# Kernel optimization log

Measured on AMD Instinct MI355X. Metric: run time of the kernel, lower is better.

## Reference

```python
import jax, jax.numpy as jnp
import numpy as np

SQN = 3      # hardcoded recurrence depth
ATT_H = 256  # hardcoded attention hidden size
STRIDE = 16  # segment length (hardcoded expand(-1,16,-1))


def setup_inputs() -> dict:
    key = jax.random.key(0)
    ks = jax.random.split(key, 12)
    B, Cin, H, V = 64, 512, 512, 512

    def w(k, shape, fan_in):
        return jax.random.normal(k, shape, jnp.float32) / np.sqrt(fan_in).astype(np.float32)

    return {
        "visual_input": jax.random.normal(ks[0], (B, Cin, V), jnp.float32),
        "text_feature": jax.random.normal(ks[1], (B, H), jnp.float32),
        # weights stored [in, out] (transposed vs torch nn.Linear)
        "vis_conv_w": w(ks[2], (Cin, H), Cin),   # 1x1 Conv1d == linear over channels
        "vis_conv_b": jnp.zeros((H,), jnp.float32),
        "glob_w": w(ks[3], (SQN, H, H), H),      # 3 distinct global_emb linears
        "glob_b": jnp.zeros((SQN, H), jnp.float32),
        "guide_w": w(ks[4], (2 * H, H), 2 * H),
        "guide_b": jnp.zeros((H,), jnp.float32),
        "att1_w": w(ks[5], (H, ATT_H), H),
        "att1_b": jnp.zeros((ATT_H,), jnp.float32),
        "att2_w": w(ks[6], (H, ATT_H), H),
        "att2_b": jnp.zeros((ATT_H,), jnp.float32),
        "att3_w": w(ks[7], (ATT_H, 1), ATT_H),
        "att3_b": jnp.zeros((1,), jnp.float32),
        "out_conv_w": w(ks[8], (H, H), H),       # 1x1 Conv1d
        "out_conv_b": jnp.zeros((H,), jnp.float32),
        "text_w": w(ks[9], (H, H), H),
        "text_b": jnp.zeros((H,), jnp.float32),
    }


def reference(visual_input, text_feature, vis_conv_w, vis_conv_b, glob_w, glob_b,
              guide_w, guide_b, att1_w, att1_b, att2_w, att2_b, att3_w, att3_b,
              out_conv_w, out_conv_b, text_w, text_b):
    B, Cin, V = visual_input.shape
    H = vis_conv_w.shape[1]
    S = V // STRIDE  # number of segments

    # vis_conv (1x1) + relu: [B, H, V]
    vis_h = jax.nn.relu(jnp.einsum('bcv,ch->bhv', visual_input, vis_conv_w)
                        + vis_conv_b[None, :, None])
    # split into segments: [B, S, T=16, H]
    vis_seg = vis_h.reshape(B, H, S, STRIDE).transpose(0, 2, 3, 1)
    # AvgPool1d(kernel=stride) == per-segment mean: [B, S, H]
    avg_seg = vis_seg.mean(axis=2)
    # text projection: [B, H]
    text_att = text_feature @ text_w + text_b

    # precompute att_fn2(vis_seg): [B, S, T, ATT_H] (loop-invariant)
    att2_pre = jnp.einsum('bsth,ha->bsta', vis_seg, att2_w) + att2_b

    prev_se = jnp.zeros((B, S, H), vis_seg.dtype)
    se_list, att_list = [], []
    for m in range(SQN):  # fixed 3-step recurrence, distinct weights per step
        v_n = jnp.einsum('bsh,hk->bsk', avg_seg, glob_w[m]) + glob_b[m]
        # guide_emb (Linear+ReLU) followed by an outer relu == single relu
        g_n = jax.nn.relu(jnp.concatenate([v_n, prev_se], axis=-1) @ guide_w + guide_b)
        att = jnp.tanh((g_n @ att1_w + att1_b)[:, :, None, :] + att2_pre)  # [B,S,T,A]
        att = att @ att3_w + att3_b                                        # [B,S,T,1]
        att = jax.nn.softmax(att, axis=2)  # softmax over the 16 frames
        prev_se = jnp.sum(vis_seg * att, axis=2)  # [B, S, H]
        se_list.append(prev_se)
        att_list.append(att)

    vis_for_att = jnp.stack(se_list, axis=2)  # [B, S, 3, H]
    fuse_att = jax.nn.softmax(jnp.einsum('bsmh,bh->bsm', vis_for_att, text_att), axis=2)
    vis_new = jnp.einsum('bsmh,bsm->bsh', vis_for_att, fuse_att)  # [B, S, H]

    # vis_out_conv (1x1) + relu over stacked segments: [B, H, S]
    vis_out = jax.nn.relu(jnp.einsum('bsh,hk->bks', vis_new, out_conv_w)
                          + out_conv_b[None, :, None])
    att_out = jnp.concatenate(att_list, axis=3)  # [B, S, 16, 3]
    return vis_out, att_out
```

## Files before the change

### kernel.cpp

```cpp
#include <hip/hip_runtime.h>

#define B_   64
#define CIN_ 512
#define H_   512
#define V_   512
#define S_   32
#define T_   16
#define A_   256
#define SQN_ 3
#define BS_  2048

typedef float  f32x4  __attribute__((ext_vector_type(4)));
typedef float  f32x2  __attribute__((ext_vector_type(2)));
typedef short  short8 __attribute__((ext_vector_type(8)));
typedef short  short4v __attribute__((ext_vector_type(4)));
typedef unsigned int uint4v __attribute__((ext_vector_type(4)));

__device__ __forceinline__ unsigned short f2bf(float f) {
    union { float f; unsigned int u; } v; v.f = f;
    unsigned int u = v.u;
    unsigned int r = (u + 0x7fffu + ((u >> 16) & 1u)) >> 16;
    return (unsigned short)r;
}
__device__ __forceinline__ float bf2f(unsigned short h) {
    union { unsigned int u; float f; } v; v.u = ((unsigned int)h) << 16;
    return v.f;
}

__device__ __forceinline__ void gload16(const void* g, void* l) {
    __builtin_amdgcn_global_load_lds(
        (const __attribute__((address_space(1))) unsigned int*)g,
        (__attribute__((address_space(3))) unsigned int*)l,
        16, 0, 0);
}

__global__ __launch_bounds__(256) void prep_kernel(
    const float* __restrict__ visual, const float* __restrict__ vis_conv_w,
    const float* __restrict__ att2_w, const float* __restrict__ guide_w,
    const float* __restrict__ att1_w, const float* __restrict__ out_conv_w,
    const float* __restrict__ glob_w, const float* __restrict__ text_feature,
    const float* __restrict__ text_w, const float* __restrict__ text_b,
    const float* __restrict__ glob_b, const float* __restrict__ guide_b,
    unsigned short* __restrict__ visT, unsigned short* __restrict__ wT_visconv,
    unsigned short* __restrict__ wT_att2, unsigned short* __restrict__ wT_guide,
    unsigned short* __restrict__ wT_att1, unsigned short* __restrict__ wT_out,
    unsigned short* __restrict__ glob_bf, float* __restrict__ text_part,
    float* __restrict__ bcomb)
{
    __shared__ __align__(16) char smem[32768];
    const int id  = blockIdx.x;
    const int tid = threadIdx.x;

    if (id < 128) {
        const int nt = id & 7, kc = id >> 3;
        const int n0 = nt * 64, kbase = kc * 32;
        float* Ts = (float*)smem;
        float* Ws = (float*)smem + 64 * 33;
        {
            const int m = tid >> 2, kk = (tid & 3) * 8;
            #pragma unroll
            for (int c = 0; c < 8; c += 4)
                *(f32x4*)&Ts[m * 33 + kk + c] =
                    *(const f32x4*)&text_feature[m * 512 + kbase + kk + c];
            const int kr = tid >> 3, nn = (tid & 7) * 8;
            #pragma unroll
            for (int c = 0; c < 8; c += 4)
                *(f32x4*)&Ws[kr * 65 + nn + c] =
                    *(const f32x4*)&text_w[(long long)(kbase + kr) * 512 + n0 + nn + c];
        }
        __syncthreads();
        const int tm = (tid >> 4) * 4, tn = (tid & 15) * 4;
        float acc[4][4] = {};
        for (int k = 0; k < 32; k++) {
            float a[4], b2[4];
            #pragma unroll
            for (int i = 0; i < 4; i++) a[i] = Ts[(tm + i) * 33 + k];
            #pragma unroll
            for (int j = 0; j < 4; j++) b2[j] = Ws[k * 65 + tn + j];
            #pragma unroll
            for (int i = 0; i < 4; i++)
                #pragma unroll
                for (int j = 0; j < 4; j++) acc[i][j] += a[i] * b2[j];
        }
        #pragma unroll
        for (int i = 0; i < 4; i++)
            #pragma unroll
            for (int j = 0; j < 4; j++)
                text_part[kc * (64 * 512) + (tm + i) * 512 + n0 + tn + j] =
                    acc[i][j] + (kc == 0 ? text_b[n0 + tn + j] : 0.0f);
        return;
    }
    if (id < 131) {
        const int m = id - 128;
        const int j2 = tid * 2;
        float a0 = guide_b[j2], a1 = guide_b[j2 + 1];
        const float* gb = glob_b + m * 512;
        #pragma unroll 8
        for (int k = 0; k < 512; k++) {
            const float g = gb[k];
            f32x2 w = *(const f32x2*)&guide_w[(long long)k * 512 + j2];
            a0 += g * w[0];
            a1 += g * w[1];
        }
        f32x2 o = {a0, a1};
        *(f32x2*)&bcomb[m * 512 + j2] = o;
        return;
    }
    if (id < 227) {
        const int base = (id - 131) * 8192 + tid * 4;
        #pragma unroll
        for (int it = 0; it < 8; it++) {
            f32x4 v = *(const f32x4*)&glob_w[base + it * 1024];
            short4v o;
            #pragma unroll
            for (int c = 0; c < 4; c++) o[c] = (short)f2bf(v[c]);
            *(short4v*)&glob_bf[base + it * 1024] = o;
        }
        return;
    }

    if (id >= 547) {
        const int q = id - 547;
        const int b = q >> 5, tile = q & 31;
        const int k0 = (tile >> 2) << 6;
        const int v0 = (tile & 3) << 7;
        const float* src = visual + (long long)b * 262144;
        unsigned short* dst = visT + (long long)b * 262144;
        float* tl = (float*)smem;

        const int wave = tid >> 6, lane = tid & 63;
        #pragma unroll
        for (int i = 0; i < 8; i++) {
            const int r2 = wave * 16 + i * 2;
            gload16(&src[(long long)(k0 + r2 + (lane >> 5)) * 512 + v0 + (lane & 31) * 4],
                    &tl[r2 * 128]);
        }
        __syncthreads();

        const int kl = (tid & 7) * 8;
        const int vb = tid >> 3;
        #pragma unroll
        for (int jv = 0; jv < 4; jv++) {
            const int v = vb + jv * 32;
            short8 o;
            #pragma unroll
            for (int i = 0; i < 8; i++)
                o[i] = (short)f2bf(tl[(kl + i) * 128 + v]);
            *(short8*)&dst[(long long)(v0 + v) * 512 + k0 + kl] = o;
        }
        return;
    }

    const float* src; unsigned short* dst; int Kd, Nd, tile;
    if (id < 291)      { tile = id - 227; src = vis_conv_w; dst = wT_visconv; Kd = 512;  Nd = 512; }
    else if (id < 323) { tile = id - 291; src = att2_w;     dst = wT_att2;    Kd = 512;  Nd = 256; }
    else if (id < 451) { tile = id - 323; src = guide_w;    dst = wT_guide;   Kd = 1024; Nd = 512; }
    else if (id < 483) { tile = id - 451; src = att1_w;     dst = wT_att1;    Kd = 512;  Nd = 256; }
    else               { tile = id - 483; src = out_conv_w; dst = wT_out;     Kd = 512;  Nd = 512; }

    unsigned int* tl = (unsigned int*)smem;
    const int xw = Nd >> 6;
    const int n0 = (tile % xw) << 6, k0 = (tile / xw) << 6;
    {
        const int r = tid >> 4;
        const int c4 = (tid & 15) * 4;
        #pragma unroll
        for (int j = 0; j < 4; j++) {
            const int row = j * 16 + r;
            f32x4 v = *(const f32x4*)&src[(long long)(k0 + row) * Nd + n0 + c4];
            #pragma unroll
            for (int c2 = 0; c2 < 4; c2++)
                tl[row * 65 + c4 + c2] = f2bf(v[c2]);
        }
    }
    __syncthreads();
    {
        const int v = tid >> 2, cq = (tid & 3) * 16;
        short8 o0, o1;
        #pragma unroll
        for (int j = 0; j < 8; j++) o0[j] = (short)tl[(cq + j) * 65 + v];
        #pragma unroll
        for (int j = 0; j < 8; j++) o1[j] = (short)tl[(cq + 8 + j) * 65 + v];
        *(short8*)&dst[(long long)(n0 + v) * Kd + k0 + cq] = o0;
        *(short8*)&dst[(long long)(n0 + v) * Kd + k0 + cq + 8] = o1;
    }
}

template <int BM, int BN, bool RELU, bool OUT_BF16, int OUT_MODE, bool ACC_INIT>
__device__ __forceinline__ void gemm_body(
    char* pool, int bid, int nwg,
    const unsigned short* __restrict__ A, long long aBatch, int lda,
    const unsigned short* __restrict__ Bt, long long bBatch, int ldb,
    const float* __restrict__ bias, long long biasBatch,
    const float* __restrict__ Cinit, int ldci,
    void* __restrict__ C, long long cBatch, int ldc,
    void* __restrict__ C2, unsigned short* __restrict__ avg_out,
    int M, int N, int K)
{
    constexpr int WM = BM / 2, WN = BN / 2;
    constexpr int FI = WM / 16, FJ = WN / 16;
    constexpr bool CT_EN  = (OUT_MODE != 1);
    constexpr bool CT_F32 = CT_EN && ((OUT_MODE == 0 && !OUT_BF16) || OUT_MODE == 3);
    constexpr int  CTS    = CT_F32 ? (BN + 4) : (BN + 8);
    constexpr int  KLOOP_B = (2 * BM * 32 + 2 * BN * 32) * 2;
    constexpr int  CT_B    = CT_EN ? (BM * CTS * (CT_F32 ? 4 : 2)) : 0;
    constexpr int  MAIN_B  = (KLOOP_B > CT_B ? KLOOP_B : CT_B);
    unsigned short* As = (unsigned short*)pool;
    unsigned short* Bs = As + 2 * BM * 32;
    float* avgl = (float*)(pool + MAIN_B);

    const int q8 = nwg >> 3, r8 = nwg & 7;
    const int xcd = bid & 7, lid = bid >> 3;
    const int logical = (xcd < r8 ? xcd * (q8 + 1)
                                  : r8 * (q8 + 1) + (xcd - r8) * q8) + lid;

    const int ntiles = N / BN;
    const int tilesPerBatch = (M / BM) * ntiles;
    const int batch = logical / tilesPerBatch;
    const int t     = logical % tilesPerBatch;
    const int tm0 = (t / ntiles) * BM;
    const int tn0 = (t % ntiles) * BN;
    const unsigned short* Ab = A + (long long)batch * aBatch;
    const unsigned short* Bb = Bt + (long long)batch * bBatch;

    const int tid  = threadIdx.x;
    const int lane = tid & 63;
    const int wave = tid >> 6;
    const int wm = (wave >> 1) * WM;
    const int wn = (wave & 1) * WN;
    const int lr = lane & 15;
    const int lk = (lane >> 4) * 8;
    const int rsub = lane >> 2;
    const int g8   = (lane & 3) * 8;

    auto stage = [&](int buf, int k0) {
        #pragma unroll
        for (int i = 0; i < BM / 64; i++) {
            const int rbase = wave * (BM / 4) + i * 16;
            gload16(&Ab[(long long)(tm0 + rbase + rsub) * lda + k0 + g8],
                    &As[buf * (BM * 32) + rbase * 32]);
        }
        #pragma unroll
        for (int i = 0; i < BN / 64; i++) {
            const int rbase = wave * (BN / 4) + i * 16;
            gload16(&Bb[(long long)(tn0 + rbase + rsub) * ldb + k0 + g8],
                    &Bs[buf * (BN * 32) + rbase * 32]);
        }
    };

    f32x4 acc[FI][FJ] = {};
    const int nk = K >> 5;

    stage(0, 0);
    __syncthreads();
    int cur = 0;
    for (int kt = 0; kt < nk; kt++) {
        if (kt + 1 < nk) stage(cur ^ 1, (kt + 1) << 5);
        const unsigned short* Ac = As + cur * (BM * 32);
        const unsigned short* Bc = Bs + cur * (BN * 32);
        short8 a[FI], b[FJ];
        #pragma unroll
        for (int i = 0; i < FI; i++)
            a[i] = *(const short8*)&Ac[(wm + i * 16 + lr) * 32 + lk];
        #pragma unroll
        for (int j = 0; j < FJ; j++)
            b[j] = *(const short8*)&Bc[(wn + j * 16 + lr) * 32 + lk];
        #pragma unroll
        for (int i = 0; i < FI; i++)
            #pragma unroll
            for (int j = 0; j < FJ; j++)
                acc[i][j] = __builtin_amdgcn_mfma_f32_16x16x32_bf16(
                    a[i], b[j], acc[i][j], 0, 0, 0);
        if (kt + 1 < nk) { __syncthreads(); cur ^= 1; }
    }

    const int erow = (lane >> 4) * 4;
    const int ecol = lane & 15;

    if constexpr (OUT_MODE == 1) {
        #pragma unroll
        for (int i = 0; i < FI; i++) {
            #pragma unroll
            for (int j = 0; j < FJ; j++) {
                const int gcol = tn0 + wn + j * 16 + ecol;
                const float bv = bias ? bias[gcol] : 0.0f;
                const int grow0 = tm0 + wm + i * 16 + erow;
                const int bb = grow0 >> 5, ss = grow0 & 31;
                f32x4 o;
                #pragma unroll
                for (int r = 0; r < 4; r++) o[r] = fmaxf(acc[i][j][r] + bv, 0.0f);
                *(f32x4*)&((float*)C)[(long long)bb * (H_ * S_) + gcol * S_ + ss] = o;
            }
        }
        return;
    } else {
        __syncthreads();
        unsigned short* CTh = (unsigned short*)pool;
        float*          CTf = (float*)pool;

        #pragma unroll
        for (int i = 0; i < FI; i++) {
            #pragma unroll
            for (int j = 0; j < FJ; j++) {
                const int lcol = wn + j * 16 + ecol;
                const int gcol = tn0 + lcol;
                const float bv = bias ? bias[(long long)batch * biasBatch + gcol] : 0.0f;
                float csum = 0.0f;
                #pragma unroll
                for (int r = 0; r < 4; r++) {
                    const int lrow = wm + i * 16 + erow + r;
                    float v = acc[i][j][r] + bv;
                    if (ACC_INIT) v += Cinit[(long long)(tm0 + lrow) * ldci + gcol];
                    if (RELU) v = fmaxf(v, 0.0f);
                    if constexpr (CT_F32) CTf[lrow * CTS + lcol] = v;
                    else                  CTh[lrow * CTS + lcol] = f2bf(v);
                    if constexpr (OUT_MODE == 2) csum += v;
                }
                if constexpr (OUT_MODE == 2) {
                    csum += __shfl_xor(csum, 16, 64);
                    csum += __shfl_xor(csum, 32, 64);
                    if (lane < 16)
                        avgl[((wm >> 4) + i) * BN + wn + j * 16 + lane] = csum;
                }
            }
        }
        __syncthreads();

        if constexpr (CT_F32) {
            constexpr int ITERS = (BM * BN) / 1024;
            #pragma unroll
            for (int it = 0; it < ITERS; it++) {
                const int flat = it * 1024 + tid * 4;
                const int row = flat / BN, col = flat % BN;
                f32x4 vv = *(const f32x4*)&CTf[row * CTS + col];
                if constexpr (OUT_MODE == 3) {
                    if (batch == 0) {
                        short4v p;
                        #pragma unroll
                        for (int c = 0; c < 4; c++) p[c] = (short)f2bf(fmaxf(vv[c], 0.0f));
                        *(short4v*)&((unsigned short*)C2)[(long long)(tm0 + row) * ldc + tn0 + col] = p;
                    } else {
                        *(f32x4*)&((float*)C)[(long long)(batch - 1) * cBatch +
                                              (long long)(tm0 + row) * ldc + tn0 + col] = vv;
                    }
                } else {
                    *(f32x4*)&((float*)C)[(long long)batch * cBatch +
                                          (long long)(tm0 + row) * ldc + tn0 + col] = vv;
                }
            }
        } else {
            constexpr int ITERS = (BM * BN) / 2048;
            #pragma unroll
            for (int it = 0; it < ITERS; it++) {
                const int flat = it * 2048 + tid * 8;
                const int row = flat / BN, col = flat % BN;
                short8 vv = *(const short8*)&CTh[row * CTS + col];
                *(short8*)&((unsigned short*)C)[(long long)batch * cBatch +
                                                (long long)(tm0 + row) * ldc + tn0 + col] = vv;
            }
        }

        if constexpr (OUT_MODE == 2) {
            const int s = tid >> 5, hq = (tid & 31) * 4;
            short4v pk;
            #pragma unroll
            for (int c = 0; c < 4; c++)
                pk[c] = (short)f2bf(avgl[s * BN + hq + c] * (1.0f / 16.0f));
            *(short4v*)&avg_out[((long long)batch * 32 + (tm0 >> 4) + s) * H_ + tn0 + hq] = pk;
        }
    }
}

template <int BM, int BN, bool RELU, bool OUT_BF16, int OUT_MODE, bool ACC_INIT>
__global__ __launch_bounds__(256) void mfma_gemm(
    const unsigned short* A, long long aBatch, int lda,
    const unsigned short* Bt, long long bBatch, int ldb,
    const float* bias, long long biasBatch,
    const float* Cinit, int ldci,
    void* C, long long cBatch, int ldc,
    void* C2, unsigned short* avg_out,
    int M, int N, int K)
{
    constexpr bool CT_EN  = (OUT_MODE != 1);
    constexpr bool CT_F32 = CT_EN && ((OUT_MODE == 0 && !OUT_BF16) || OUT_MODE == 3);
    constexpr int  CTS    = CT_F32 ? (BN + 4) : (BN + 8);
    constexpr int  KLOOP_B = (2 * BM * 32 + 2 * BN * 32) * 2;
    constexpr int  CT_B    = CT_EN ? (BM * CTS * (CT_F32 ? 4 : 2)) : 0;
    constexpr int  MAIN_B  = (KLOOP_B > CT_B ? KLOOP_B : CT_B);
    constexpr int  AVG_B   = (OUT_MODE == 2) ? (BM / 16) * BN * 4 : 0;
    __shared__ __align__(16) char pool[MAIN_B + AVG_B];
    gemm_body<BM, BN, RELU, OUT_BF16, OUT_MODE, ACC_INIT>(
        pool, blockIdx.x, gridDim.x,
        A, aBatch, lda, Bt, bBatch, ldb, bias, biasBatch, Cinit, ldci,
        C, cBatch, ldc, C2, avg_out, M, N, K);
}

__global__ __launch_bounds__(256) void wcomb_visconv_kernel(
    const unsigned short* wT_guide, const unsigned short* glob_bf,
    unsigned short* WcombT,
    const unsigned short* visT, const unsigned short* wT_visconv,
    const float* vis_conv_b, unsigned short* vis_seg, unsigned short* avg)
{
    __shared__ __align__(16) char pool[40960];
    if (blockIdx.x < 192) {
        gemm_body<64, 64, false, true, 0, false>(pool, blockIdx.x, 192,
            wT_guide, 0, 1024,
            glob_bf, (long long)H_ * H_, H_,
            nullptr, 0, nullptr, 0,
            WcombT, (long long)H_ * H_, H_, nullptr, nullptr, H_, H_, H_);
    } else {
        gemm_body<128, 128, true, true, 2, false>(pool, blockIdx.x - 192, 1024,
            visT, (long long)V_ * CIN_, CIN_,
            wT_visconv, 0, CIN_,
            vis_conv_b, 0, nullptr, 0,
            vis_seg, (long long)V_ * H_, H_, nullptr, avg, V_, H_, CIN_);
    }
}

__global__ __launch_bounds__(256) void att2_p_kernel(
    const unsigned short* vis_seg, const unsigned short* wT_att2,
    const float* att2_b, unsigned short* att2_pre,
    const unsigned short* avg, const unsigned short* WcombT,
    const float* bcomb, float* P, unsigned short* gbuf)
{
    __shared__ __align__(16) char pool[40960];
    if (blockIdx.x < 512) {
        gemm_body<128, 128, false, true, 0, false>(pool, blockIdx.x, 512,
            vis_seg, (long long)V_ * H_, H_,
            wT_att2, 0, H_,
            att2_b, 0, nullptr, 0,
            att2_pre, (long long)V_ * A_, A_, nullptr, nullptr, V_, A_, H_);
    } else {
        gemm_body<64, 64, false, false, 3, false>(pool, blockIdx.x - 512, 768,
            avg, 0, H_,
            WcombT, (long long)H_ * H_, H_,
            bcomb, H_, nullptr, 0,
            P, (long long)BS_ * H_, H_, gbuf, nullptr, BS_, H_, H_);
    }
}

template <bool LAST>
__global__ __launch_bounds__(256) void fused_att_kernel(
    const float* __restrict__ att1,
    const unsigned short* __restrict__ att2_pre,
    const float* __restrict__ att3_w,
    const float* __restrict__ att3_b,
    const unsigned short* __restrict__ vis_seg,
    float* __restrict__ se_m,
    unsigned short* __restrict__ pse,
    float* __restrict__ att_out, int m,
    const float* __restrict__ se_base,
    const float* __restrict__ text_part,
    const float* __restrict__ text_b,
    unsigned short* __restrict__ vis_new)
{
    const int bs = blockIdx.x, tid = threadIdx.x;
    const int wave = tid >> 6, lane = tid & 63;
    __shared__ float logits[T_], wts[T_];
    __shared__ float part[3][512];
    __shared__ float redf[4][3];
    __shared__ float swf[3];
    __shared__ float tsh[512];

    if constexpr (LAST) {
        const int b = bs >> 5;
        for (int h = tid; h < 512; h += 256) {
            float s = text_b[h];
            #pragma unroll
            for (int p = 0; p < 16; p++)
                s += text_part[p * (64 * 512) + b * 512 + h];
            tsh[h] = s;
        }
    }

    f32x4 a1r = *(const f32x4*)&att1[(long long)bs * A_ + lane * 4];
    f32x4 w3r = *(const f32x4*)&att3_w[lane * 4];

    #pragma unroll
    for (int qq = 0; qq < 4; qq++) {
        const int t = wave * 4 + qq;
        short4v ap = *(const short4v*)&att2_pre[(long long)(bs * T_ + t) * A_ + lane * 4];
        float x = 0.f;
        #pragma unroll
        for (int c = 0; c < 4; c++)
            x += tanhf(a1r[c] + bf2f((unsigned short)ap[c])) * w3r[c];
        #pragma unroll
        for (int off = 32; off > 0; off >>= 1) x += __shfl_down(x, off, 64);
        if (lane == 0) logits[t] = x + att3_b[0];
    }
    __syncthreads();
    if (tid == 0) {
        float mx = logits[0];
        #pragma unroll
        for (int t = 1; t < T_; t++) mx = fmaxf(mx, logits[t]);
        float s = 0.f;
        #pragma unroll
        for (int t = 0; t < T_; t++) { float e = expf(logits[t] - mx); wts[t] = e; s += e; }
        float inv = 1.0f / s;
        #pragma unroll
        for (int t = 0; t < T_; t++) wts[t] *= inv;
    }
    __syncthreads();
    if (tid < T_) att_out[bs * (T_ * SQN_) + tid * SQN_ + m] = wts[tid];

    const int slot = tid & 63, quarter = tid >> 6;
    float s[8] = {};
    #pragma unroll
    for (int tt = 0; tt < 4; tt++) {
        const int t = quarter * 4 + tt;
        short8 vv = *(const short8*)&vis_seg[(long long)(bs * T_ + t) * H_ + slot * 8];
        const float w = wts[t];
        #pragma unroll
        for (int c = 0; c < 8; c++) s[c] += bf2f((unsigned short)vv[c]) * w;
    }
    if (quarter) {
        #pragma unroll
        for (int c = 0; c < 8; c++) part[quarter - 1][slot * 8 + c] = s[c];
    }
    __syncthreads();
    if (quarter == 0) {
        #pragma unroll
        for (int c = 0; c < 8; c++)
            s[c] += part[0][slot * 8 + c] + part[1][slot * 8 + c] + part[2][slot * 8 + c];
    }

    if constexpr (!LAST) {
        if (quarter == 0) {
            f32x4 o0 = {s[0], s[1], s[2], s[3]};
            f32x4 o1 = {s[4], s[5], s[6], s[7]};
            *(f32x4*)&se_m[(long long)bs * H_ + slot * 8] = o0;
            *(f32x4*)&se_m[(long long)bs * H_ + slot * 8 + 4] = o1;
            short8 p;
            #pragma unroll
            for (int c = 0; c < 8; c++) p[c] = (short)f2bf(s[c]);
            *(short8*)&pse[(long long)bs * H_ + slot * 8] = p;
        }
    } else {
        const float* se0 = se_base + (long long)bs * H_;
        const float* se1 = se_base + (long long)BS_ * H_ + (long long)bs * H_;

        float p0 = 0.f, p1 = 0.f, p2 = 0.f;
        {
            const int h2 = tid * 2;
            float t0 = tsh[h2], t1 = tsh[h2 + 1];
            p0 = se0[h2] * t0 + se0[h2 + 1] * t1;
            p1 = se1[h2] * t0 + se1[h2 + 1] * t1;
        }
        if (quarter == 0) {
            #pragma unroll
            for (int c = 0; c < 8; c++) p2 += s[c] * tsh[slot * 8 + c];
        }
        #pragma unroll
        for (int off = 32; off > 0; off >>= 1) {
            p0 += __shfl_down(p0, off, 64);
            p1 += __shfl_down(p1, off, 64);
            p2 += __shfl_down(p2, off, 64);
        }
        if (lane == 0) { redf[wave][0] = p0; redf[wave][1] = p1; redf[wave][2] = p2; }
        __syncthreads();
        if (tid == 0) {
            float d0 = redf[0][0] + redf[1][0] + redf[2][0] + redf[3][0];
            float d1 = redf[0][1] + redf[1][1] + redf[2][1] + redf[3][1];
            float d2 = redf[0][2] + redf[1][2] + redf[2][2] + redf[3][2];
            float mx = fmaxf(d0, fmaxf(d1, d2));
            float e0 = expf(d0 - mx), e1 = expf(d1 - mx), e2 = expf(d2 - mx);
            float inv = 1.0f / (e0 + e1 + e2);
            swf[0] = e0 * inv; swf[1] = e1 * inv; swf[2] = e2 * inv;
        }
        __syncthreads();
        if (quarter == 0) {
            const float w0 = swf[0], w1 = swf[1], w2 = swf[2];
            short8 p;
            #pragma unroll
            for (int c = 0; c < 8; c++) {
                const int h = slot * 8 + c;
                p[c] = (short)f2bf(w0 * se0[h] + w1 * se1[h] + w2 * s[c]);
            }
            *(short8*)&vis_new[(long long)bs * H_ + slot * 8] = p;
        }
    }
}

extern "C" void kernel_launch(void* const* d_in, const int* in_sizes, int n_in,
                              void* d_out, int out_size, void* d_ws, size_t ws_size,
                              hipStream_t stream)
{
    const float* visual       = (const float*)d_in[0];
    const float* text_feature = (const float*)d_in[1];
    const float* vis_conv_w   = (const float*)d_in[2];
    const float* vis_conv_b   = (const float*)d_in[3];
    const float* glob_w       = (const float*)d_in[4];
    const float* glob_b       = (const float*)d_in[5];
    const float* guide_w      = (const float*)d_in[6];
    const float* guide_b      = (const float*)d_in[7];
    const float* att1_w       = (const float*)d_in[8];
    const float* att1_b       = (const float*)d_in[9];
    const float* att2_w       = (const float*)d_in[10];
    const float* att2_b       = (const float*)d_in[11];
    const float* att3_w       = (const float*)d_in[12];
    const float* att3_b       = (const float*)d_in[13];
    const float* out_conv_w   = (const float*)d_in[14];
    const float* out_conv_b   = (const float*)d_in[15];
    const float* text_w       = (const float*)d_in[16];
    const float* text_b       = (const float*)d_in[17];
    float* out = (float*)d_out;
    float* att_out = out + (B_ * H_ * S_);

    char* base = (char*)d_ws;
    unsigned short* visT     = (unsigned short*)(base + 0);
    unsigned short* vis_seg  = (unsigned short*)(base + 33554432);
    unsigned short* att2_pre = (unsigned short*)(base + 67108864);
    float*          se       = (float*)(base + 100663296);
    float*          P        = (float*)(base + 113246208);
    unsigned short* pse      = (unsigned short*)(base + 125829120);
    unsigned short* gbuf     = (unsigned short*)(base + 127926272);
    float*          att1buf  = (float*)(base + 130023424);
    unsigned short* avg      = (unsigned short*)(base + 132120576);
    unsigned short* vis_new  = (unsigned short*)(base + 134348800);
    char*           wbase    = base + 136445952;
    unsigned short* wT_visconv = (unsigned short*)(wbase + 0);
    unsigned short* wT_att2    = (unsigned short*)(wbase + 524288);
    unsigned short* wT_guide   = (unsigned short*)(wbase + 786432);
    unsigned short* wT_att1    = (unsigned short*)(wbase + 1835008);
    unsigned short* wT_out     = (unsigned short*)(wbase + 2097152);
    unsigned short* glob_bf    = (unsigned short*)(wbase + 2621440);
    unsigned short* WcombT     = (unsigned short*)(wbase + 4194304);
    float*          bcomb      = (float*)(wbase + 5767168);
    float*          text_part  = (float*)(wbase + 6291456);

    prep_kernel<<<dim3(2595), 256, 0, stream>>>(
        visual, vis_conv_w, att2_w, guide_w, att1_w, out_conv_w, glob_w,
        text_feature, text_w, text_b, glob_b, guide_b,
        visT, wT_visconv, wT_att2, wT_guide, wT_att1, wT_out,
        glob_bf, text_part, bcomb);

    wcomb_visconv_kernel<<<dim3(192 + 1024), 256, 0, stream>>>(
        wT_guide, glob_bf, WcombT,
        visT, wT_visconv, vis_conv_b, vis_seg, avg);

    att2_p_kernel<<<dim3(512 + 768), 256, 0, stream>>>(
        vis_seg, wT_att2, att2_b, att2_pre,
        avg, WcombT, bcomb, P, gbuf);

    for (int m = 0; m < SQN_; m++) {
        if (m > 0) {
            mfma_gemm<64, 64, true, true, 0, true><<<dim3(256), 256, 0, stream>>>(
                pse, 0, H_,
                wT_guide + 512, 0, 1024,
                nullptr, 0, P + (long long)(m - 1) * BS_ * H_, H_,
                gbuf, 0, H_, nullptr, nullptr, BS_, H_, H_);
        }
        mfma_gemm<64, 64, false, false, 0, false><<<dim3(128), 256, 0, stream>>>(
            gbuf, 0, H_,
            wT_att1, 0, H_,
            att1_b, 0, nullptr, 0,
            att1buf, 0, A_, nullptr, nullptr, BS_, A_, H_);
        if (m < SQN_ - 1) {
            fused_att_kernel<false><<<dim3(BS_), 256, 0, stream>>>(
                att1buf, att2_pre, att3_w, att3_b, vis_seg,
                se + (long long)m * BS_ * H_, pse, att_out, m,
                nullptr, nullptr, nullptr, nullptr);
        } else {
            fused_att_kernel<true><<<dim3(BS_), 256, 0, stream>>>(
                att1buf, att2_pre, att3_w, att3_b, vis_seg,
                nullptr, nullptr, att_out, m,
                se, text_part, text_b, vis_new);
        }
    }

    mfma_gemm<64, 64, true, false, 1, false><<<dim3(256), 256, 0, stream>>>(
        vis_new, 0, H_,
        wT_out, 0, H_,
        out_conv_b, 0, nullptr, 0,
        out, 0, 0, nullptr, nullptr, BS_, H_, H_);
}
```

Measured before the change: 184.1 us.

## Swizzle GEMM LDS layout, use explicit vmcnt barriers, shrink LDS, fast tanh

The GEMM staging XOR-swizzles the 16-byte chunk index within each 32-element K row, and the fragment reads apply the matching swizzle. The goal is fewer LDS bank conflicts when loading MFMA operands. __syncthreads is replaced by an explicit vmcnt(0) wait plus s_barrier with a sched_barrier, and the shared pools in two kernels are trimmed, which may allow more resident workgroups. In the attention kernel, tanhf becomes an exp/rcp approximation, trading a little accuracy for fewer instructions.

```diff
diff --git a/kernel.cpp b/kernel.cpp
--- a/kernel.cpp
+++ b/kernel.cpp
@@ -27,11 +27,21 @@
     return v.f;
 }
 
+__device__ __forceinline__ float fast_tanhf(float x) {
+    float cx = fminf(fmaxf(x, -15.0f), 15.0f);
+    float e  = __expf(2.0f * cx);
+    return (e - 1.0f) * __builtin_amdgcn_rcpf(e + 1.0f);
+}
+
 __device__ __forceinline__ void gload16(const void* g, void* l) {
     __builtin_amdgcn_global_load_lds(
         (const __attribute__((address_space(1))) unsigned int*)g,
         (__attribute__((address_space(3))) unsigned int*)l,
         16, 0, 0);
+}
+
+template <int N> __device__ __forceinline__ void waitv() {
+    asm volatile("s_waitcnt vmcnt(%0)" :: "n"(N) : "memory");
 }
 
 __global__ __launch_bounds__(256) void prep_kernel(
@@ -202,7 +212,7 @@
     constexpr bool CT_EN  = (OUT_MODE != 1);
     constexpr bool CT_F32 = CT_EN && ((OUT_MODE == 0 && !OUT_BF16) || OUT_MODE == 3);
     constexpr int  CTS    = CT_F32 ? (BN + 4) : (BN + 8);
-    constexpr int  KLOOP_B = (2 * BM * 32 + 2 * BN * 32) * 2;
+    constexpr int  KLOOP_B = 2 * (BM * 32 + BN * 32) * 2;
     constexpr int  CT_B    = CT_EN ? (BM * CTS * (CT_F32 ? 4 : 2)) : 0;
     constexpr int  MAIN_B  = (KLOOP_B > CT_B ? KLOOP_B : CT_B);
     unsigned short* As = (unsigned short*)pool;
@@ -231,19 +241,20 @@
     const int lr = lane & 15;
     const int lk = (lane >> 4) * 8;
     const int rsub = lane >> 2;
-    const int g8   = (lane & 3) * 8;
+    const int g8s = ((lane & 3) ^ ((lane >> 3) & 3)) * 8;
+    const int lks = lk ^ (((lr >> 1) & 3) << 3);
 
     auto stage = [&](int buf, int k0) {
         #pragma unroll
         for (int i = 0; i < BM / 64; i++) {
             const int rbase = wave * (BM / 4) + i * 16;
-            gload16(&Ab[(long long)(tm0 + rbase + rsub) * lda + k0 + g8],
+            gload16(&Ab[(long long)(tm0 + rbase + rsub) * lda + k0 + g8s],
                     &As[buf * (BM * 32) + rbase * 32]);
         }
         #pragma unroll
         for (int i = 0; i < BN / 64; i++) {
             const int rbase = wave * (BN / 4) + i * 16;
-            gload16(&Bb[(long long)(tn0 + rbase + rsub) * ldb + k0 + g8],
+            gload16(&Bb[(long long)(tn0 + rbase + rsub) * ldb + k0 + g8s],
                     &Bs[buf * (BN * 32) + rbase * 32]);
         }
     };
@@ -252,26 +263,35 @@
     const int nk = K >> 5;
 
     stage(0, 0);
-    __syncthreads();
+    waitv<0>();
+    __builtin_amdgcn_s_barrier();
+
     int cur = 0;
     for (int kt = 0; kt < nk; kt++) {
         if (kt + 1 < nk) stage(cur ^ 1, (kt + 1) << 5);
+
         const unsigned short* Ac = As + cur * (BM * 32);
         const unsigned short* Bc = Bs + cur * (BN * 32);
         short8 a[FI], b[FJ];
         #pragma unroll
         for (int i = 0; i < FI; i++)
-            a[i] = *(const short8*)&Ac[(wm + i * 16 + lr) * 32 + lk];
+            a[i] = *(const short8*)&Ac[(wm + i * 16 + lr) * 32 + lks];
         #pragma unroll
         for (int j = 0; j < FJ; j++)
-            b[j] = *(const short8*)&Bc[(wn + j * 16 + lr) * 32 + lk];
+            b[j] = *(const short8*)&Bc[(wn + j * 16 + lr) * 32 + lks];
         #pragma unroll
         for (int i = 0; i < FI; i++)
             #pragma unroll
             for (int j = 0; j < FJ; j++)
                 acc[i][j] = __builtin_amdgcn_mfma_f32_16x16x32_bf16(
                     a[i], b[j], acc[i][j], 0, 0, 0);
-        if (kt + 1 < nk) { __syncthreads(); cur ^= 1; }
+
+        if (kt + 1 < nk) {
+            __builtin_amdgcn_sched_barrier(0);
+            waitv<0>();
+            __builtin_amdgcn_s_barrier();
+            cur ^= 1;
+        }
     }
 
     const int erow = (lane >> 4) * 4;
@@ -384,7 +404,7 @@
     constexpr bool CT_EN  = (OUT_MODE != 1);
     constexpr bool CT_F32 = CT_EN && ((OUT_MODE == 0 && !OUT_BF16) || OUT_MODE == 3);
     constexpr int  CTS    = CT_F32 ? (BN + 4) : (BN + 8);
-    constexpr int  KLOOP_B = (2 * BM * 32 + 2 * BN * 32) * 2;
+    constexpr int  KLOOP_B = 2 * (BM * 32 + BN * 32) * 2;
     constexpr int  CT_B    = CT_EN ? (BM * CTS * (CT_F32 ? 4 : 2)) : 0;
     constexpr int  MAIN_B  = (KLOOP_B > CT_B ? KLOOP_B : CT_B);
     constexpr int  AVG_B   = (OUT_MODE == 2) ? (BM / 16) * BN * 4 : 0;
@@ -401,7 +421,7 @@
     const unsigned short* visT, const unsigned short* wT_visconv,
     const float* vis_conv_b, unsigned short* vis_seg, unsigned short* avg)
 {
-    __shared__ __align__(16) char pool[40960];
+    __shared__ __align__(16) char pool[38912];
     if (blockIdx.x < 192) {
         gemm_body<64, 64, false, true, 0, false>(pool, blockIdx.x, 192,
             wT_guide, 0, 1024,
@@ -423,7 +443,7 @@
     const unsigned short* avg, const unsigned short* WcombT,
     const float* bcomb, float* P, unsigned short* gbuf)
 {
-    __shared__ __align__(16) char pool[40960];
+    __shared__ __align__(16) char pool[34816];
     if (blockIdx.x < 512) {
         gemm_body<128, 128, false, true, 0, false>(pool, blockIdx.x, 512,
             vis_seg, (long long)V_ * H_, H_,
@@ -483,7 +503,7 @@
         float x = 0.f;
         #pragma unroll
         for (int c = 0; c < 4; c++)
-            x += tanhf(a1r[c] + bf2f((unsigned short)ap[c])) * w3r[c];
+            x += fast_tanhf(a1r[c] + bf2f((unsigned short)ap[c])) * w3r[c];
         #pragma unroll
         for (int off = 32; off > 0; off >>= 1) x += __shfl_down(x, off, 64);
         if (lane == 0) logits[t] = x + att3_b[0];
```

Result: no change. 181.3 us (-1.5%).
